# Performance work log

Measured on AMD Instinct MI355X. Metric: run time of the kernel, lower is better.

The kernel has to match this reference:

```python
import jax, jax.numpy as jnp
import numpy as np

NUM_HEADS = 4

def _proj(x, w, b):
    # Conv1d kernel_size=1 == pointwise linear over channels: [B, Cin, N] -> [B, Cout, N]
    return jnp.einsum('oi,bin->bon', w, x) + b[None, :, None]

def setup_inputs() -> dict:
    key = jax.random.key(0)
    ks = jax.random.split(key, 11)
    B, D, N = 8, 256, 2048
    inp = {
        'query': jax.random.normal(ks[0], (B, D, N), jnp.float32),
        'key':   jax.random.normal(ks[1], (B, D, N), jnp.float32),
        'value': jax.random.normal(ks[2], (B, D, N), jnp.float32),
        'w_q': jax.random.normal(ks[3], (D, D), jnp.float32) * (1.0 / np.sqrt(D)),
        'b_q': jax.random.normal(ks[4], (D,), jnp.float32) * 0.02,
        'w_k': jax.random.normal(ks[5], (D, D), jnp.float32) * (1.0 / np.sqrt(D)),
        'b_k': jax.random.normal(ks[6], (D,), jnp.float32) * 0.02,
        'w_v': jax.random.normal(ks[7], (D, D), jnp.float32) * (1.0 / np.sqrt(D)),
        'b_v': jax.random.normal(ks[8], (D,), jnp.float32) * 0.02,
        'w_m': jax.random.normal(ks[9], (D, D), jnp.float32) * (1.0 / np.sqrt(D)),
        'b_m': jax.random.normal(ks[10], (D,), jnp.float32) * 0.02,
    }
    return inp

def reference(query, key, value, w_q, b_q, w_k, b_k, w_v, b_v, w_m, b_m):
    B, D, N = query.shape
    H = NUM_HEADS
    d = D // H  # head dim (outer slot of channel split, matching torch .view)
    q = _proj(query, w_q, b_q).reshape(B, d, H, N)
    k = _proj(key,   w_k, b_k).reshape(B, d, H, N)
    v = _proj(value, w_v, b_v).reshape(B, d, H, N)
    scale = jnp.asarray(1.0 / np.sqrt(d), q.dtype)
    scores = jnp.einsum('bdhn,bdhm->bhnm', q, k) * scale  # [B,H,N,N]
    prob = jax.nn.softmax(scores, axis=-1)
    x = jnp.einsum('bhnm,bdhm->bdhn', prob, v)            # [B,d,H,N]
    out = _proj(x.reshape(B, D, N), w_m, b_m)             # [B,D,N]
    return out
```

## Files before the change

kernel.cpp:

```cpp
#include <hip/hip_runtime.h>
#include <cstdint>
#include <cstddef>

typedef unsigned short u16;
typedef unsigned int   u32;
typedef __attribute__((ext_vector_type(4))) float f32x4;
typedef __attribute__((ext_vector_type(16))) float f32x16;
typedef __attribute__((ext_vector_type(8))) short bf16x8;
typedef __attribute__((ext_vector_type(2))) u32 u32x2;
typedef __attribute__((ext_vector_type(4))) u32 u32x4;

#define DEVI static __device__ __forceinline__
#define MFMA16(a,b,c) __builtin_amdgcn_mfma_f32_16x16x32_bf16((a),(b),(c),0,0,0)
#define MFMA32(a,b,c) __builtin_amdgcn_mfma_f32_32x32x16_bf16((a),(b),(c),0,0,0)
#define BAR()   __builtin_amdgcn_s_barrier()
#define CFENCE() asm volatile("" ::: "memory")

DEVI u16 f2b(float f) {
  u32 u = __builtin_bit_cast(u32, f);
  u32 r = u + 0x7fffu + ((u >> 16) & 1u);
  return (u16)(r >> 16);
}

DEVI u32 pkbf(float a, float b) {
  u32 r;
  asm("v_cvt_pk_bf16_f32 %0, %1, %2" : "=v"(r) : "v"(a), "v"(b));
  return r;
}

DEVI void load_lds16(const void* g, void* l) {
  __builtin_amdgcn_global_load_lds(
      (const __attribute__((address_space(1))) u32*)g,
      (__attribute__((address_space(3))) u32*)l, 16, 0, 0);
}

DEVI int perm_o(int o) { return 4 * (o & 63) + (o >> 6); }

__global__ __launch_bounds__(256) void k_pre(
    const float* __restrict__ q, const float* __restrict__ k, const float* __restrict__ v,
    const float* __restrict__ wq, const float* __restrict__ wk,
    const float* __restrict__ wv, const float* __restrict__ wm,
    const float* __restrict__ bq, const float* __restrict__ bk, const float* __restrict__ bv,
    u16* __restrict__ xq, u16* __restrict__ xk, u16* __restrict__ xv,
    u16* __restrict__ WQ, u16* __restrict__ WK, u16* __restrict__ WV, u16* __restrict__ WM,
    float* __restrict__ BQ, float* __restrict__ BK, float* __restrict__ BV)
{
  __shared__ u16 tile[64][68];
  int blk = blockIdx.x, t = threadIdx.x;
  if (blk < 3072) {
    const int N = 2048, D = 256;
    int x = blk & 31, y = (blk >> 5) & 3, z = blk >> 7;
    int n0 = x * 64, c0 = y * 64;
    int b = z & 7, which = z >> 3;
    const float* src = (which == 0 ? q : which == 1 ? k : v) + (size_t)b * D * N;
    u16* dst = (which == 0 ? xq : which == 1 ? xk : xv) + (size_t)b * N * D;
    int cl = t >> 4, ng = t & 15;
#pragma unroll
    for (int cc = 0; cc < 4; ++cc) {
      int c = cl + 16 * cc;
      f32x4 val = *(const f32x4*)&src[(size_t)(c0 + c) * N + n0 + ng * 4];
#pragma unroll
      for (int j = 0; j < 4; ++j) tile[c][ng * 4 + j] = f2b(val[j]);
    }
    __syncthreads();
    int n = t & 63, cq = t >> 6;
    union { u16 s[16]; u32x4 v4[2]; } pk;
#pragma unroll
    for (int j = 0; j < 16; ++j) pk.s[j] = tile[cq * 16 + j][n];
    u32x4* o = (u32x4*)&dst[(size_t)(n0 + n) * D + c0 + cq * 16];
    o[0] = pk.v4[0];
    o[1] = pk.v4[1];
  } else {
    int p = blk - 3072;
    int row = p & 255, m = p >> 8;
    if (m == 0)      WQ[row * 256 + t] = f2b(wq[perm_o(row) * 256 + t]);
    else if (m == 1) WK[row * 256 + t] = f2b(wk[perm_o(row) * 256 + t]);
    else if (m == 2) WV[row * 256 + t] = f2b(wv[perm_o(row) * 256 + t]);
    else if (m == 3) WM[row * 256 + t] = f2b(wm[row * 256 + perm_o(t)]);
    else if (row == 0) {
      BQ[t] = bq[perm_o(t)];
      BK[t] = bk[perm_o(t)];
      BV[t] = bv[perm_o(t)];
    }
  }
}

__global__ __launch_bounds__(256, 4) void k_gemm3(
    const u16* __restrict__ XQ, const u16* __restrict__ XK, const u16* __restrict__ XV,
    const u16* __restrict__ WQm, const u16* __restrict__ WKm, const u16* __restrict__ WVm,
    const float* __restrict__ BQ, const float* __restrict__ BK, const float* __restrict__ BV,
    u16* __restrict__ QT, u16* __restrict__ KT, u16* __restrict__ VW)
{
  __shared__ u16 lA[2][64 * 64];
  __shared__ u16 lB[2][64 * 64];
  int gid = blockIdx.x, t = threadIdx.x;
  int wk = gid >> 10, rem = gid & 1023;
  int b = rem >> 7;
  int bx, by, epi;
  const u16 *Ab, *Bb;
  const float* bias;
  u16* outp;
  if (wk < 2) {
    bx = rem & 31; by = (rem >> 5) & 3;
    Ab = (wk ? XK : XQ) + (size_t)b * (2048 * 256) + (size_t)bx * 64 * 256;
    Bb = (wk ? WKm : WQm) + (size_t)by * 64 * 256;
    bias = wk ? BK : BQ;
    outp = (wk ? KT : QT) + (size_t)b * (4L * 2048 * 64);
    epi = 0;
  } else {
    bx = rem & 3; by = (rem >> 2) & 31;
    Ab = WVm + (size_t)bx * 64 * 256;
    Bb = XV + (size_t)b * (2048 * 256) + (size_t)by * 64 * 256;
    bias = BV;
    outp = VW + (size_t)b * (256L * 2048);
    epi = 1;
  }
  int l = t & 63, w = t >> 6, g = l >> 4, col = l & 15;
  int wr = w >> 1, wc = w & 1;
  f32x4 acc[2][2] = {};
  u32 sOf[2], sDs[2];
#pragma unroll
  for (int j = 0; j < 2; ++j) {
    int ci = t + 256 * j;
    int r = ci >> 3, c = ci & 7;
    sOf[j] = (u32)(r * 512 + ((c ^ (r & 7)) << 4));
    sDs[j] = (u32)(ci * 16);
  }
  auto stage = [&](int buf, int k0) {
#pragma unroll
    for (int j = 0; j < 2; ++j) {
      load_lds16((const char*)Ab + k0 * 2 + sOf[j], (char*)lA[buf] + sDs[j]);
      load_lds16((const char*)Bb + k0 * 2 + sOf[j], (char*)lB[buf] + sDs[j]);
    }
  };
  stage(0, 0);
  for (int s = 0; s < 4; ++s) {
    int cur = s & 1;
    if (s < 3) {
      stage(cur ^ 1, (s + 1) * 64);
      asm volatile("s_waitcnt vmcnt(4)" ::: "memory");
    } else {
      asm volatile("s_waitcnt vmcnt(0)" ::: "memory");
    }
    BAR(); CFENCE();
#pragma unroll
    for (int kc = 0; kc < 2; ++kc) {
      bf16x8 af[2], bfr[2];
#pragma unroll
      for (int mt = 0; mt < 2; ++mt) {
        int row = wr * 32 + mt * 16 + col;
        af[mt] = *(const bf16x8*)((const char*)lA[cur] + row * 128 + (((kc * 4 + g) ^ (row & 7)) << 4));
      }
#pragma unroll
      for (int nt = 0; nt < 2; ++nt) {
        int row = wc * 32 + nt * 16 + col;
        bfr[nt] = *(const bf16x8*)((const char*)lB[cur] + row * 128 + (((kc * 4 + g) ^ (row & 7)) << 4));
      }
#pragma unroll
      for (int mt = 0; mt < 2; ++mt)
#pragma unroll
        for (int nt = 0; nt < 2; ++nt)
          acc[mt][nt] = MFMA16(af[mt], bfr[nt], acc[mt][nt]);
    }
    if (s < 3) { CFENCE(); BAR(); }
  }
  if (epi == 0) {
#pragma unroll
    for (int nt = 0; nt < 2; ++nt) {
      int op = by * 64 + wc * 32 + nt * 16 + col;
      int hh = op >> 6, ii = op & 63;
      float bv = bias[op];
#pragma unroll
      for (int mt = 0; mt < 2; ++mt) {
        int nbase = bx * 64 + wr * 32 + mt * 16 + g * 4;
#pragma unroll
        for (int r = 0; r < 4; ++r)
          outp[((size_t)(hh * 2048 + nbase + r)) * 64 + ii] = f2b(acc[mt][nt][r] + bv);
      }
    }
  } else {
#pragma unroll
    for (int mt = 0; mt < 2; ++mt)
#pragma unroll
      for (int r = 0; r < 4; ++r) {
        int row = bx * 64 + wr * 32 + mt * 16 + g * 4 + r;
        float bv = bias[row];
#pragma unroll
        for (int nt = 0; nt < 2; ++nt) {
          int cn = by * 64 + wc * 32 + nt * 16 + col;
          outp[(size_t)row * 2048 + cn] = f2b(acc[mt][nt][r] + bv);
        }
      }
  }
}

__global__ __launch_bounds__(256, 4) void k_gemmM(
    const u16* __restrict__ A,
    const u16* __restrict__ Bm, long sB,
    const float* __restrict__ bias,
    float* __restrict__ out, long sOut)
{
  __shared__ u16 lA[2][64 * 64];
  __shared__ u16 lB[2][64 * 64];
  int t = threadIdx.x, b = blockIdx.z;
  const u16* Ab = A + (size_t)blockIdx.x * 64 * 256;
  const u16* Bb = Bm + (size_t)b * sB + (size_t)blockIdx.y * 64 * 256;
  int l = t & 63, w = t >> 6, g = l >> 4, col = l & 15;
  int wr = w >> 1, wc = w & 1;
  f32x4 acc[2][2] = {};
  u32 sOf[2], sDs[2];
#pragma unroll
  for (int j = 0; j < 2; ++j) {
    int ci = t + 256 * j;
    int r = ci >> 3, c = ci & 7;
    sOf[j] = (u32)(r * 512 + ((c ^ (r & 7)) << 4));
    sDs[j] = (u32)(ci * 16);
  }
  auto stage = [&](int buf, int k0) {
#pragma unroll
    for (int j = 0; j < 2; ++j) {
      load_lds16((const char*)Ab + k0 * 2 + sOf[j], (char*)lA[buf] + sDs[j]);
      load_lds16((const char*)Bb + k0 * 2 + sOf[j], (char*)lB[buf] + sDs[j]);
    }
  };
  stage(0, 0);
  for (int s = 0; s < 4; ++s) {
    int cur = s & 1;
    if (s < 3) {
      stage(cur ^ 1, (s + 1) * 64);
      asm volatile("s_waitcnt vmcnt(4)" ::: "memory");
    } else {
      asm volatile("s_waitcnt vmcnt(0)" ::: "memory");
    }
    BAR(); CFENCE();
#pragma unroll
    for (int kc = 0; kc < 2; ++kc) {
      bf16x8 af[2], bfr[2];
#pragma unroll
      for (int mt = 0; mt < 2; ++mt) {
        int row = wr * 32 + mt * 16 + col;
        af[mt] = *(const bf16x8*)((const char*)lA[cur] + row * 128 + (((kc * 4 + g) ^ (row & 7)) << 4));
      }
#pragma unroll
      for (int nt = 0; nt < 2; ++nt) {
        int row = wc * 32 + nt * 16 + col;
        bfr[nt] = *(const bf16x8*)((const char*)lB[cur] + row * 128 + (((kc * 4 + g) ^ (row & 7)) << 4));
      }
#pragma unroll
      for (int mt = 0; mt < 2; ++mt)
#pragma unroll
        for (int nt = 0; nt < 2; ++nt)
          acc[mt][nt] = MFMA16(af[mt], bfr[nt], acc[mt][nt]);
    }
    if (s < 3) { CFENCE(); BAR(); }
  }
  float* o = out + (size_t)b * sOut;
#pragma unroll
  for (int mt = 0; mt < 2; ++mt)
#pragma unroll
    for (int r = 0; r < 4; ++r) {
      int row = blockIdx.x * 64 + wr * 32 + mt * 16 + g * 4 + r;
      float bv = bias[row];
#pragma unroll
      for (int nt = 0; nt < 2; ++nt) {
        int cn = blockIdx.y * 64 + wc * 32 + nt * 16 + col;
        o[(size_t)row * 2048 + cn] = acc[mt][nt][r] + bv;
      }
    }
}

__global__ __launch_bounds__(256, 2) void k_attn(
    const u16* __restrict__ Qt, const u16* __restrict__ Kt,
    const u16* __restrict__ Vw, u16* __restrict__ Xws)
{
  __shared__ u16 stg[4][2][4096];
  const float SC2 = 0.18033688011112042f;
  int t = threadIdx.x, l = t & 63;
  int w = t >> 6;
  int hi = l >> 5, col = l & 31;
  int lin = blockIdx.x;
  int xcd = lin & 7, j = lin >> 3;
  int bh = xcd * 4 + (j >> 4);
  int nb = j & 15;
  int b = bh >> 2, hh = bh & 3;
  const u16* Qb = Qt + ((size_t)(b * 4 + hh) * 2048) * 64;
  const u16* Kb = Kt + ((size_t)(b * 4 + hh) * 2048) * 64;
  const u16* Vb = Vw + ((size_t)(b * 256 + hh * 64)) * 2048;
  int nq = nb * 128 + w * 32 + col;

  bf16x8 qf[4];
#pragma unroll
  for (int ks = 0; ks < 4; ++ks)
    qf[ks] = *(const bf16x8*)&Qb[(size_t)nq * 64 + ks * 16 + hi * 8];

  u32 kSrc[2], vSrc[2], sDst[2];
#pragma unroll
  for (int jj = 0; jj < 2; ++jj) {
    int ci = t + 256 * jj;
    int r = ci >> 3, c = ci & 7;
    u32 sw = (u32)((c ^ ((r >> 1) & 7)) << 4);
    kSrc[jj] = (u32)(r * 128) + sw;
    vSrc[jj] = (u32)(r * 4096) + sw;
    sDst[jj] = (u32)(ci * 16);
  }
  u32 offC[4];
#pragma unroll
  for (int ks = 0; ks < 4; ++ks)
    offC[ks] = (u32)(((2 * ks + hi) ^ ((col >> 1) & 7)) << 4);
  u32 colb = (u32)(col * 128);

  f32x16 xac0 = {}, xac1 = {};
  float psum = 0.0f, m_run = 0.0f;

  auto stage = [&](int buf, int tile) {
    const char* kb = (const char*)Kb + (size_t)tile * 8192;
    const char* vb = (const char*)Vb + (size_t)tile * 128;
#pragma unroll
    for (int jj = 0; jj < 2; ++jj)
      load_lds16(kb + kSrc[jj], (char*)stg[buf][0] + sDst[jj]);
#pragma unroll
    for (int jj = 0; jj < 2; ++jj)
      load_lds16(vb + vSrc[jj], (char*)stg[buf][1] + sDst[jj]);
  };

  auto do_qk = [&](int buf, f32x16& s0, f32x16& s1) {
    const char* kK = (const char*)stg[buf][0] + colb;
    __builtin_amdgcn_s_setprio(1);
#pragma unroll
    for (int ks = 0; ks < 4; ++ks) {
      bf16x8 kf0 = *(const bf16x8*)(kK + offC[ks]);
      bf16x8 kf1 = *(const bf16x8*)(kK + 4096 + offC[ks]);
      s0 = MFMA32(kf0, qf[ks], s0);
      s1 = MFMA32(kf1, qf[ks], s1);
    }
    __builtin_amdgcn_s_setprio(0);
  };

  auto do_sm_pv = [&](int buf, const f32x16& s0, const f32x16& s1) {
    bf16x8 pf[4];
    float ps = 0.0f;
#pragma unroll
    for (int mt = 0; mt < 2; ++mt) {
      const f32x16& sc = mt ? s1 : s0;
      float p[16];
#pragma unroll
      for (int r = 0; r < 16; ++r) {
        p[r] = __builtin_amdgcn_exp2f(__builtin_fmaf(sc[r], SC2, -m_run));
        ps += p[r];
      }
      u32 A0 = pkbf(p[0],  p[1]),  B0 = pkbf(p[2],  p[3]);
      u32 A1 = pkbf(p[4],  p[5]),  B1 = pkbf(p[6],  p[7]);
      u32 A2 = pkbf(p[8],  p[9]),  B2 = pkbf(p[10], p[11]);
      u32 A3 = pkbf(p[12], p[13]), B3 = pkbf(p[14], p[15]);
      asm("v_permlane32_swap_b32 %0, %1" : "+v"(A0), "+v"(A1));
      asm("v_permlane32_swap_b32 %0, %1" : "+v"(B0), "+v"(B1));
      asm("v_permlane32_swap_b32 %0, %1" : "+v"(A2), "+v"(A3));
      asm("v_permlane32_swap_b32 %0, %1" : "+v"(B2), "+v"(B3));
      union { u32 u[4]; bf16x8 v; } f0, f1;
      f0.u[0] = A0; f0.u[1] = B0; f0.u[2] = A1; f0.u[3] = B1;
      f1.u[0] = A2; f1.u[1] = B2; f1.u[2] = A3; f1.u[3] = B3;
      pf[mt * 2 + 0] = f0.v;
      pf[mt * 2 + 1] = f1.v;
    }
    psum += ps;
    const char* kV = (const char*)stg[buf][1] + colb;
    __builtin_amdgcn_s_setprio(1);
#pragma unroll
    for (int S = 0; S < 4; ++S) {
      bf16x8 vf0 = *(const bf16x8*)(kV + offC[S]);
      bf16x8 vf1 = *(const bf16x8*)(kV + 4096 + offC[S]);
      xac0 = MFMA32(vf0, pf[S], xac0);
      xac1 = MFMA32(vf1, pf[S], xac1);
    }
    __builtin_amdgcn_s_setprio(0);
  };

  stage(0, 0);
  stage(1, 1);
  asm volatile("s_waitcnt vmcnt(4)" ::: "memory");
  BAR(); CFENCE();
  f32x16 sA0 = {}, sA1 = {};
  do_qk(0, sA0, sA1);
  stage(2, 2);

  for (int it = 0; it < 31; ++it) {
    if (__any(psum > 16777216.0f)) {
      const float ds = 5.9604644775390625e-8f;
      xac0 *= ds; xac1 *= ds; psum *= ds;
      m_run += 24.0f;
    }
    if (it < 30) {
      asm volatile("s_waitcnt vmcnt(4)" ::: "memory");
    } else {
      asm volatile("s_waitcnt vmcnt(0)" ::: "memory");
    }
    BAR(); CFENCE();
    if (it + 3 <= 31) stage((it + 3) & 3, it + 3);
    f32x16 sB0 = {}, sB1 = {};
    do_qk((it + 1) & 3, sB0, sB1);
    do_sm_pv(it & 3, sA0, sA1);
    sA0 = sB0; sA1 = sB1;
  }
  if (__any(psum > 16777216.0f)) {
    const float ds = 5.9604644775390625e-8f;
    xac0 *= ds; xac1 *= ds; psum *= ds;
    m_run += 24.0f;
  }
  do_sm_pv(31 & 3, sA0, sA1);

  psum += __shfl_xor(psum, 32);
  float inv = 1.0f / psum;
  u16* Ob = Xws + (size_t)b * 2048 * 256 + (size_t)nq * 256 + hh * 64;
#pragma unroll
  for (int it2 = 0; it2 < 2; ++it2) {
    const f32x16& xa = it2 ? xac1 : xac0;
#pragma unroll
    for (int rq = 0; rq < 4; ++rq) {
      float v0 = xa[4 * rq + 0] * inv;
      float v1 = xa[4 * rq + 1] * inv;
      float v2 = xa[4 * rq + 2] * inv;
      float v3 = xa[4 * rq + 3] * inv;
      u32x2 w2; w2[0] = pkbf(v0, v1); w2[1] = pkbf(v2, v3);
      *(u32x2*)&Ob[it2 * 32 + 8 * rq + 4 * hi] = w2;
    }
  }
}

extern "C" void kernel_launch(void* const* d_in, const int* in_sizes, int n_in,
                              void* d_out, int out_size, void* d_ws, size_t ws_size,
                              hipStream_t stream)
{
  const float* q_in = (const float*)d_in[0];
  const float* k_in = (const float*)d_in[1];
  const float* v_in = (const float*)d_in[2];
  const float* w_q  = (const float*)d_in[3];
  const float* b_q  = (const float*)d_in[4];
  const float* w_k  = (const float*)d_in[5];
  const float* b_k  = (const float*)d_in[6];
  const float* w_v  = (const float*)d_in[7];
  const float* b_v  = (const float*)d_in[8];
  const float* w_m  = (const float*)d_in[9];
  const float* b_m  = (const float*)d_in[10];

  char* ws = (char*)d_ws;
  u16* XT_Q = (u16*)(ws + 0);
  u16* XT_K = (u16*)(ws + 8388608);
  u16* XT_V = (u16*)(ws + 16777216);
  u16* QT   = (u16*)(ws + 25165824);
  u16* KT   = (u16*)(ws + 33554432);
  u16* VW   = (u16*)(ws + 41943040);
  u16* WQ   = (u16*)(ws + 50331648);
  u16* WK   = (u16*)(ws + 50462720);
  u16* WV   = (u16*)(ws + 50593792);
  u16* WM   = (u16*)(ws + 50724864);
  float* BQ = (float*)(ws + 50855936);
  float* BK = (float*)(ws + 50856960);
  float* BV = (float*)(ws + 50857984);

  k_pre<<<dim3(4352), 256, 0, stream>>>(q_in, k_in, v_in, w_q, w_k, w_v, w_m,
                                        b_q, b_k, b_v, XT_Q, XT_K, XT_V,
                                        WQ, WK, WV, WM, BQ, BK, BV);
  k_gemm3<<<dim3(3072), 256, 0, stream>>>(XT_Q, XT_K, XT_V, WQ, WK, WV,
                                          BQ, BK, BV, QT, KT, VW);
  k_attn<<<dim3(512), 256, 0, stream>>>(QT, KT, VW, XT_Q);
  k_gemmM<<<dim3(4, 32, 8), 256, 0, stream>>>(WM, XT_Q, 2048L * 256, b_m,
                                              (float*)d_out, 256L * 2048);
}
```

Measured before the change: 99.76 us.

## Restructure attention kernel into single-wave blocks with 32-key tiles and double buffering

The attention kernel moves from 256-thread blocks (4 waves sharing 64-key K/V tiles, 4-stage pipeline with barriers) to 64-thread single-wave blocks, each handling 32 queries over 32-key tiles with a 2-stage LDS buffer. No block barrier is needed any more, and the QK/softmax/PV software pipelining across tiles is dropped in favour of a straightforward per-tile sequence. The grid grows to 2048 blocks. In exchange there is no K/V sharing across waves, so global/L2 traffic for K and V rises roughly fourfold, and the loop runs twice as many iterations with less MFMA overlap.

```diff
diff --git a/kernel.cpp b/kernel.cpp
--- a/kernel.cpp
+++ b/kernel.cpp
@@ -269,144 +269,127 @@
     }
 }
 
-__global__ __launch_bounds__(256, 2) void k_attn(
+__global__ __launch_bounds__(64, 2) void k_attn(
     const u16* __restrict__ Qt, const u16* __restrict__ Kt,
     const u16* __restrict__ Vw, u16* __restrict__ Xws)
 {
-  __shared__ u16 stg[4][2][4096];
+  __shared__ u16 stg[2][2][2048];
   const float SC2 = 0.18033688011112042f;
-  int t = threadIdx.x, l = t & 63;
-  int w = t >> 6;
-  int hi = l >> 5, col = l & 31;
+  int t = threadIdx.x;
+  int hi = t >> 5, col = t & 31;
   int lin = blockIdx.x;
   int xcd = lin & 7, j = lin >> 3;
-  int bh = xcd * 4 + (j >> 4);
-  int nb = j & 15;
+  int bh = xcd * 4 + (j >> 6), nb = j & 63;
   int b = bh >> 2, hh = bh & 3;
   const u16* Qb = Qt + ((size_t)(b * 4 + hh) * 2048) * 64;
   const u16* Kb = Kt + ((size_t)(b * 4 + hh) * 2048) * 64;
   const u16* Vb = Vw + ((size_t)(b * 256 + hh * 64)) * 2048;
-  int nq = nb * 128 + w * 32 + col;
+  int nq = nb * 32 + col;
 
   bf16x8 qf[4];
 #pragma unroll
   for (int ks = 0; ks < 4; ++ks)
     qf[ks] = *(const bf16x8*)&Qb[(size_t)nq * 64 + ks * 16 + hi * 8];
 
-  u32 kSrc[2], vSrc[2], sDst[2];
-#pragma unroll
-  for (int jj = 0; jj < 2; ++jj) {
-    int ci = t + 256 * jj;
-    int r = ci >> 3, c = ci & 7;
-    u32 sw = (u32)((c ^ ((r >> 1) & 7)) << 4);
-    kSrc[jj] = (u32)(r * 128) + sw;
-    vSrc[jj] = (u32)(r * 4096) + sw;
-    sDst[jj] = (u32)(ci * 16);
-  }
-  u32 offC[4];
+  u32 kSrc[4], vSrc[4], sDst[4];
+#pragma unroll
+  for (int j2 = 0; j2 < 4; ++j2) {
+    int c = t + 64 * j2;
+    int rk = c >> 3, ck = c & 7;
+    kSrc[j2] = (u32)(rk * 128 + ((ck ^ ((rk >> 1) & 7)) << 4));
+    int rv = c >> 2, cv = c & 3;
+    vSrc[j2] = (u32)(rv * 4096 + ((cv ^ ((rv >> 3) & 3)) << 4));
+    sDst[j2] = (u32)(c * 16);
+  }
+  u32 offK[4];
 #pragma unroll
   for (int ks = 0; ks < 4; ++ks)
-    offC[ks] = (u32)(((2 * ks + hi) ^ ((col >> 1) & 7)) << 4);
-  u32 colb = (u32)(col * 128);
+    offK[ks] = (u32)(((2 * ks + hi) ^ ((col >> 1) & 7)) << 4);
+  u32 offV[2];
+#pragma unroll
+  for (int S = 0; S < 2; ++S)
+    offV[S] = (u32)(((S * 2 + hi) ^ ((col >> 3) & 3)) << 4);
 
   f32x16 xac0 = {}, xac1 = {};
   float psum = 0.0f, m_run = 0.0f;
 
   auto stage = [&](int buf, int tile) {
-    const char* kb = (const char*)Kb + (size_t)tile * 8192;
-    const char* vb = (const char*)Vb + (size_t)tile * 128;
-#pragma unroll
-    for (int jj = 0; jj < 2; ++jj)
-      load_lds16(kb + kSrc[jj], (char*)stg[buf][0] + sDst[jj]);
-#pragma unroll
-    for (int jj = 0; jj < 2; ++jj)
-      load_lds16(vb + vSrc[jj], (char*)stg[buf][1] + sDst[jj]);
-  };
-
-  auto do_qk = [&](int buf, f32x16& s0, f32x16& s1) {
-    const char* kK = (const char*)stg[buf][0] + colb;
-    __builtin_amdgcn_s_setprio(1);
-#pragma unroll
-    for (int ks = 0; ks < 4; ++ks) {
-      bf16x8 kf0 = *(const bf16x8*)(kK + offC[ks]);
-      bf16x8 kf1 = *(const bf16x8*)(kK + 4096 + offC[ks]);
-      s0 = MFMA32(kf0, qf[ks], s0);
-      s1 = MFMA32(kf1, qf[ks], s1);
-    }
-    __builtin_amdgcn_s_setprio(0);
-  };
-
-  auto do_sm_pv = [&](int buf, const f32x16& s0, const f32x16& s1) {
-    bf16x8 pf[4];
-    float ps = 0.0f;
-#pragma unroll
-    for (int mt = 0; mt < 2; ++mt) {
-      const f32x16& sc = mt ? s1 : s0;
-      float p[16];
-#pragma unroll
-      for (int r = 0; r < 16; ++r) {
-        p[r] = __builtin_amdgcn_exp2f(__builtin_fmaf(sc[r], SC2, -m_run));
-        ps += p[r];
-      }
-      u32 A0 = pkbf(p[0],  p[1]),  B0 = pkbf(p[2],  p[3]);
-      u32 A1 = pkbf(p[4],  p[5]),  B1 = pkbf(p[6],  p[7]);
-      u32 A2 = pkbf(p[8],  p[9]),  B2 = pkbf(p[10], p[11]);
-      u32 A3 = pkbf(p[12], p[13]), B3 = pkbf(p[14], p[15]);
-      asm("v_permlane32_swap_b32 %0, %1" : "+v"(A0), "+v"(A1));
-      asm("v_permlane32_swap_b32 %0, %1" : "+v"(B0), "+v"(B1));
-      asm("v_permlane32_swap_b32 %0, %1" : "+v"(A2), "+v"(A3));
-      asm("v_permlane32_swap_b32 %0, %1" : "+v"(B2), "+v"(B3));
-      union { u32 u[4]; bf16x8 v; } f0, f1;
-      f0.u[0] = A0; f0.u[1] = B0; f0.u[2] = A1; f0.u[3] = B1;
-      f1.u[0] = A2; f1.u[1] = B2; f1.u[2] = A3; f1.u[3] = B3;
-      pf[mt * 2 + 0] = f0.v;
-      pf[mt * 2 + 1] = f1.v;
-    }
-    psum += ps;
-    const char* kV = (const char*)stg[buf][1] + colb;
-    __builtin_amdgcn_s_setprio(1);
-#pragma unroll
-    for (int S = 0; S < 4; ++S) {
-      bf16x8 vf0 = *(const bf16x8*)(kV + offC[S]);
-      bf16x8 vf1 = *(const bf16x8*)(kV + 4096 + offC[S]);
-      xac0 = MFMA32(vf0, pf[S], xac0);
-      xac1 = MFMA32(vf1, pf[S], xac1);
-    }
-    __builtin_amdgcn_s_setprio(0);
+    const char* kb = (const char*)(Kb + (size_t)tile * 32 * 64);
+    const char* vb = (const char*)(Vb + (size_t)tile * 32);
+#pragma unroll
+    for (int j2 = 0; j2 < 4; ++j2)
+      load_lds16(kb + kSrc[j2], (char*)stg[buf][0] + sDst[j2]);
+#pragma unroll
+    for (int j2 = 0; j2 < 4; ++j2)
+      load_lds16(vb + vSrc[j2], (char*)stg[buf][1] + sDst[j2]);
   };
 
   stage(0, 0);
   stage(1, 1);
-  asm volatile("s_waitcnt vmcnt(4)" ::: "memory");
-  BAR(); CFENCE();
-  f32x16 sA0 = {}, sA1 = {};
-  do_qk(0, sA0, sA1);
-  stage(2, 2);
-
-  for (int it = 0; it < 31; ++it) {
+  for (int it = 0; it < 64; ++it) {
+    int cur = it & 1;
     if (__any(psum > 16777216.0f)) {
       const float ds = 5.9604644775390625e-8f;
       xac0 *= ds; xac1 *= ds; psum *= ds;
       m_run += 24.0f;
     }
-    if (it < 30) {
-      asm volatile("s_waitcnt vmcnt(4)" ::: "memory");
+    if (it < 63) {
+      asm volatile("s_waitcnt vmcnt(8)" ::: "memory");
     } else {
       asm volatile("s_waitcnt vmcnt(0)" ::: "memory");
     }
-    BAR(); CFENCE();
-    if (it + 3 <= 31) stage((it + 3) & 3, it + 3);
-    f32x16 sB0 = {}, sB1 = {};
-    do_qk((it + 1) & 3, sB0, sB1);
-    do_sm_pv(it & 3, sA0, sA1);
-    sA0 = sB0; sA1 = sB1;
-  }
-  if (__any(psum > 16777216.0f)) {
-    const float ds = 5.9604644775390625e-8f;
-    xac0 *= ds; xac1 *= ds; psum *= ds;
-    m_run += 24.0f;
-  }
-  do_sm_pv(31 & 3, sA0, sA1);
+    CFENCE();
+    const char* kK = (const char*)stg[cur][0] + col * 128;
+    const char* kV = (const char*)stg[cur][1] + col * 64;
+
+    f32x16 sac = {};
+    __builtin_amdgcn_s_setprio(1);
+#pragma unroll
+    for (int ks = 0; ks < 4; ++ks) {
+      bf16x8 kf = *(const bf16x8*)(kK + offK[ks]);
+      sac = MFMA32(kf, qf[ks], sac);
+    }
+    __builtin_amdgcn_s_setprio(0);
+
+    float p[16];
+#pragma unroll
+    for (int r = 0; r < 16; ++r) {
+      p[r] = __builtin_amdgcn_exp2f(__builtin_fmaf(sac[r], SC2, -m_run));
+    }
+    psum += ((p[0] + p[1]) + (p[2] + p[3])) + ((p[4] + p[5]) + (p[6] + p[7]))
+          + ((p[8] + p[9]) + (p[10] + p[11])) + ((p[12] + p[13]) + (p[14] + p[15]));
+    u32 A0 = pkbf(p[0],  p[1]),  B0 = pkbf(p[2],  p[3]);
+    u32 A1 = pkbf(p[4],  p[5]),  B1 = pkbf(p[6],  p[7]);
+    u32 A2 = pkbf(p[8],  p[9]),  B2 = pkbf(p[10], p[11]);
+    u32 A3 = pkbf(p[12], p[13]), B3 = pkbf(p[14], p[15]);
+    asm("v_permlane32_swap_b32 %0, %1" : "+v"(A0), "+v"(A1));
+    asm("v_permlane32_swap_b32 %0, %1" : "+v"(B0), "+v"(B1));
+    asm("v_permlane32_swap_b32 %0, %1" : "+v"(A2), "+v"(A3));
+    asm("v_permlane32_swap_b32 %0, %1" : "+v"(B2), "+v"(B3));
+    union { u32 u[4]; bf16x8 v; } f0, f1;
+    f0.u[0] = A0; f0.u[1] = B0; f0.u[2] = A1; f0.u[3] = B1;
+    f1.u[0] = A2; f1.u[1] = B2; f1.u[2] = A3; f1.u[3] = B3;
+    bf16x8 pf0 = f0.v, pf1 = f1.v;
+
+    __builtin_amdgcn_s_setprio(1);
+    {
+      bf16x8 va = *(const bf16x8*)(kV + offV[0]);
+      bf16x8 vb2 = *(const bf16x8*)(kV + 2048 + offV[0]);
+      xac0 = MFMA32(va, pf0, xac0);
+      xac1 = MFMA32(vb2, pf0, xac1);
+      bf16x8 vc = *(const bf16x8*)(kV + offV[1]);
+      bf16x8 vd = *(const bf16x8*)(kV + 2048 + offV[1]);
+      xac0 = MFMA32(vc, pf1, xac0);
+      xac1 = MFMA32(vd, pf1, xac1);
+    }
+    __builtin_amdgcn_s_setprio(0);
+
+    if (it + 2 <= 63) {
+      asm volatile("s_waitcnt lgkmcnt(0)" ::: "memory");
+      __builtin_amdgcn_sched_barrier(0);
+      stage(cur, it + 2);
+    }
+  }
 
   psum += __shfl_xor(psum, 32);
   float inv = 1.0f / psum;
@@ -462,7 +445,7 @@
                                         WQ, WK, WV, WM, BQ, BK, BV);
   k_gemm3<<<dim3(3072), 256, 0, stream>>>(XT_Q, XT_K, XT_V, WQ, WK, WV,
                                           BQ, BK, BV, QT, KT, VW);
-  k_attn<<<dim3(512), 256, 0, stream>>>(QT, KT, VW, XT_Q);
+  k_attn<<<dim3(2048), 64, 0, stream>>>(QT, KT, VW, XT_Q);
   k_gemmM<<<dim3(4, 32, 8), 256, 0, stream>>>(WM, XT_Q, 2048L * 256, b_m,
                                               (float*)d_out, 256L * 2048);
 }
```

Result: slower. 124.7 us (+25.0%).
